# Optimization experiments

Hardware: AMD Instinct MI355X
Metric: run time of the kernel (lower is better)

## Reference

```python
import jax, jax.numpy as jnp
import numpy as np

NUM_NODES = 64
NUM_FEATURES = 256
OUTPUT_DIM = 256
BATCH_GRAPHS = 4096
TOTAL_ROWS = NUM_NODES * BATCH_GRAPHS


def setup_inputs() -> dict:
    key = jax.random.key(0)
    kx, kw = jax.random.split(key)
    x = jax.random.normal(kx, (TOTAL_ROWS, NUM_FEATURES), dtype=jnp.float32)
    # row i belongs to graph i // NUM_NODES (matches stride-num_nodes indexing in the module)
    batch = jnp.arange(TOTAL_ROWS, dtype=jnp.int64) // NUM_NODES
    # per-node linear weights: mlp[inode] is o3.Linear(256x0e -> 256x0e), bias-free
    W = jax.random.normal(kw, (NUM_NODES, NUM_FEATURES, OUTPUT_DIM), dtype=jnp.float32)
    return {"x": x, "batch": batch, "W": W}


def reference(x, batch, W):
    # x: [B*num_nodes, F]; W: [num_nodes, F, O]
    num_nodes, F, _ = W.shape
    B = x.shape[0] // num_nodes
    # node_features_reshape: out[b, :, inode] = x[inode + b*num_nodes] == reshape(B, num_nodes, F)
    xr = x.reshape(B, num_nodes, F)
    scale = 1.0 / jnp.sqrt(jnp.asarray(F, dtype=x.dtype))  # o3.Linear path normalization
    out = jnp.einsum("bnf,nfo->bno", xr, W) * scale  # per-node batched GEMM
    # scatter back: outs[inode + b*num_nodes] = out[b, inode] == reshape
    return out.reshape(B * num_nodes, -1)
```

## Files before the change

### kernel.cpp

```cpp
#include <hip/hip_runtime.h>
#include <stdint.h>

#define NODES   64
#define FDIM    256
#define ODIM    256
#define BGRAPH  4096
#define TROWS   (NODES * BGRAPH)

#define BM 64
#define BN 256
#define BK 32

typedef short  bf16x8  __attribute__((ext_vector_type(8)));
typedef float  floatx4 __attribute__((ext_vector_type(4)));

__device__ inline unsigned short f2bf(float f) {
    unsigned int u = __float_as_uint(f);
    return (unsigned short)((u + 0x7fffu + ((u >> 16) & 1u)) >> 16);
}

__global__ __launch_bounds__(256) void transpose_w(const float* __restrict__ W,
                                                   unsigned short* __restrict__ Wt) {
    __shared__ unsigned short t[64][65];
    const int node = blockIdx.y;
    const int tf = (blockIdx.x >> 2) << 6;
    const int to = (blockIdx.x & 3) << 6;
    const int tid = threadIdx.x;
    const float* Wn = W + node * (FDIM * ODIM);
#pragma unroll
    for (int i = 0; i < 16; ++i) {
        int flat = i * 256 + tid;
        int r = flat >> 6, c = flat & 63;
        float v = Wn[(tf + r) * ODIM + (to + c)] * 0.0625f;
        t[c][r] = f2bf(v);
    }
    __syncthreads();
    unsigned short* Wtn = Wt + node * (FDIM * ODIM);
#pragma unroll
    for (int i = 0; i < 16; ++i) {
        int flat = i * 256 + tid;
        int r = flat >> 6, c = flat & 63;
        Wtn[(to + r) * FDIM + (tf + c)] = t[r][c];
    }
}

__global__ __launch_bounds__(512, 4) void gemm_node(const float* __restrict__ x,
                                                    const unsigned short* __restrict__ Wt,
                                                    float* __restrict__ out) {
    __shared__ __align__(16) unsigned short As[BM * 256];
    __shared__ __align__(16) unsigned short Bs[2][BN * BK];

    const int bid  = blockIdx.x;
    const int xcd  = bid & 7;
    const int jj   = bid >> 3;
    const int node = xcd * 8 + (jj & 7);
    const int mblk = jj >> 3;
    const int b0   = mblk * BM;

    const int tid  = threadIdx.x;
    const int lane = tid & 63;
    const int wave = tid >> 6;
    const int wm   = wave >> 2;
    const int wn   = wave & 3;
    const int l15  = lane & 15;
    const int l4   = lane >> 4;

    const float* xblk = x + ((size_t)b0 * NODES + node) * FDIM;
    const unsigned short* wt_node = Wt + (size_t)node * (ODIM * FDIM);

#pragma unroll
    for (int j = 0; j < 2; ++j) {
        const int slot_base = (wave * 2 + j) * 64;
        const int s = slot_base + lane;
        const int o = s >> 2, c = s & 3;
        const int jg = c ^ ((o >> 1) & 3);
        const unsigned short* g = wt_node + (size_t)o * FDIM + jg * 8;
        __builtin_amdgcn_global_load_lds(
            (const __attribute__((address_space(1))) void*)g,
            (__attribute__((address_space(3))) void*)(&Bs[0][slot_base * 8]),
            16, 0, 0);
    }

#pragma unroll
    for (int i = 0; i < 8; ++i) {
        const int q = i * 512 + tid;
        const int r = q >> 6, ch = q & 63;
        const float4 v = *(const float4*)(xblk + (size_t)r * (NODES * FDIM) + ch * 4);
        ushort4 p;
        p.x = f2bf(v.x); p.y = f2bf(v.y); p.z = f2bf(v.z); p.w = f2bf(v.w);
        const int slot = (ch >> 1) ^ (r & 7);
        *(ushort4*)(&As[r * 256 + slot * 8 + (ch & 1) * 4]) = p;
    }
    __syncthreads();

    floatx4 acc[2][4] = {};

#pragma unroll
    for (int kt = 0; kt < 8; ++kt) {
        const int cur = kt & 1, nxt = cur ^ 1;

        if (kt < 7) {
            const int k1 = (kt + 1) * BK;
#pragma unroll
            for (int j = 0; j < 2; ++j) {
                const int slot_base = (wave * 2 + j) * 64;
                const int s = slot_base + lane;
                const int o = s >> 2, c = s & 3;
                const int jg = c ^ ((o >> 1) & 3);
                const unsigned short* g = wt_node + (size_t)o * FDIM + k1 + jg * 8;
                __builtin_amdgcn_global_load_lds(
                    (const __attribute__((address_space(1))) void*)g,
                    (__attribute__((address_space(3))) void*)(&Bs[nxt][slot_base * 8]),
                    16, 0, 0);
            }
        }

        bf16x8 a[2], b[4];
#pragma unroll
        for (int mi = 0; mi < 2; ++mi) {
            const int m = wm * 32 + mi * 16 + l15;
            const int slot = (kt * 4 + l4) ^ (m & 7);
            a[mi] = *(const bf16x8*)(&As[m * 256 + slot * 8]);
        }
#pragma unroll
        for (int ni = 0; ni < 4; ++ni) {
            const int n = wn * 64 + ni * 16 + l15;
            b[ni] = *(const bf16x8*)(&Bs[cur][n * 32 + (l4 ^ ((n >> 1) & 3)) * 8]);
        }

#pragma unroll
        for (int mi = 0; mi < 2; ++mi)
#pragma unroll
            for (int ni = 0; ni < 4; ++ni)
                acc[mi][ni] = __builtin_amdgcn_mfma_f32_16x16x32_bf16(a[mi], b[ni], acc[mi][ni], 0, 0, 0);

        if (kt < 7) __syncthreads();
    }

    float* outblk = out + ((size_t)b0 * NODES + node) * ODIM;
#pragma unroll
    for (int mi = 0; mi < 2; ++mi) {
        const int row_base = wm * 32 + mi * 16 + l4 * 4;
#pragma unroll
        for (int ni = 0; ni < 4; ++ni) {
            const int col = wn * 64 + ni * 16 + l15;
#pragma unroll
            for (int r = 0; r < 4; ++r) {
                outblk[(size_t)(row_base + r) * (NODES * ODIM) + col] = acc[mi][ni][r];
            }
        }
    }
}

__global__ __launch_bounds__(256) void naive_kernel(const float* __restrict__ x,
                                                    const float* __restrict__ W,
                                                    float* __restrict__ out) {
    __shared__ float xs[FDIM];
    const int row = blockIdx.x;
    const int node = row & (NODES - 1);
    const int o = threadIdx.x;
    xs[o] = x[(size_t)row * FDIM + o];
    __syncthreads();
    const float* Wn = W + (size_t)node * FDIM * ODIM;
    float s = 0.f;
#pragma unroll 8
    for (int f = 0; f < FDIM; ++f) s += xs[f] * Wn[(size_t)f * ODIM + o];
    out[(size_t)row * ODIM + o] = s * 0.0625f;
}

extern "C" void kernel_launch(void* const* d_in, const int* in_sizes, int n_in,
                              void* d_out, int out_size, void* d_ws, size_t ws_size,
                              hipStream_t stream) {
    const float* x = (const float*)d_in[0];
    const float* W = (const float*)d_in[2];
    float* out = (float*)d_out;

    const size_t wt_bytes = (size_t)NODES * ODIM * FDIM * sizeof(unsigned short);
    if (ws_size >= wt_bytes) {
        unsigned short* Wt = (unsigned short*)d_ws;
        transpose_w<<<dim3(16, NODES), 256, 0, stream>>>(W, Wt);
        gemm_node<<<dim3((BGRAPH / BM) * NODES), 512, 0, stream>>>(x, Wt, out);
    } else {
        naive_kernel<<<dim3(TROWS), 256, 0, stream>>>(x, W, out);
    }
}
```

Before: 455.6 us.

## Load W fragments directly from global into registers, drop LDS B staging

Removes the shared-memory double buffer for the weight tile. Each lane now loads its MFMA B fragments straight from global memory into registers, with an even/odd register double buffer, which also removes the per-k-step __syncthreads. This cuts LDS traffic, LDS footprint and block-wide barriers. In exchange, each wave issues many small strided global loads, and the two wm waves that share a wn column fetch the same W data redundantly (served by cache). Global latency may also be less well hidden.

```diff
diff --git a/kernel.cpp b/kernel.cpp
--- a/kernel.cpp
+++ b/kernel.cpp
@@ -48,7 +48,6 @@
                                                     const unsigned short* __restrict__ Wt,
                                                     float* __restrict__ out) {
     __shared__ __align__(16) unsigned short As[BM * 256];
-    __shared__ __align__(16) unsigned short Bs[2][BN * BK];
 
     const int bid  = blockIdx.x;
     const int xcd  = bid & 7;
@@ -68,18 +67,12 @@
     const float* xblk = x + ((size_t)b0 * NODES + node) * FDIM;
     const unsigned short* wt_node = Wt + (size_t)node * (ODIM * FDIM);
 
+    const unsigned short* bbase = wt_node + (size_t)(wn * 64 + l15) * FDIM + l4 * 8;
+
+    bf16x8 be[4], bo[4];
 #pragma unroll
-    for (int j = 0; j < 2; ++j) {
-        const int slot_base = (wave * 2 + j) * 64;
-        const int s = slot_base + lane;
-        const int o = s >> 2, c = s & 3;
-        const int jg = c ^ ((o >> 1) & 3);
-        const unsigned short* g = wt_node + (size_t)o * FDIM + jg * 8;
-        __builtin_amdgcn_global_load_lds(
-            (const __attribute__((address_space(1))) void*)g,
-            (__attribute__((address_space(3))) void*)(&Bs[0][slot_base * 8]),
-            16, 0, 0);
-    }
+    for (int ni = 0; ni < 4; ++ni)
+        be[ni] = *(const bf16x8*)(bbase + ni * 16 * FDIM);
 
 #pragma unroll
     for (int i = 0; i < 8; ++i) {
@@ -97,44 +90,30 @@
 
 #pragma unroll
     for (int kt = 0; kt < 8; ++kt) {
-        const int cur = kt & 1, nxt = cur ^ 1;
-
         if (kt < 7) {
             const int k1 = (kt + 1) * BK;
 #pragma unroll
-            for (int j = 0; j < 2; ++j) {
-                const int slot_base = (wave * 2 + j) * 64;
-                const int s = slot_base + lane;
-                const int o = s >> 2, c = s & 3;
-                const int jg = c ^ ((o >> 1) & 3);
-                const unsigned short* g = wt_node + (size_t)o * FDIM + k1 + jg * 8;
-                __builtin_amdgcn_global_load_lds(
-                    (const __attribute__((address_space(1))) void*)g,
-                    (__attribute__((address_space(3))) void*)(&Bs[nxt][slot_base * 8]),
-                    16, 0, 0);
+            for (int ni = 0; ni < 4; ++ni) {
+                bf16x8 v = *(const bf16x8*)(bbase + ni * 16 * FDIM + k1);
+                if (kt & 1) be[ni] = v; else bo[ni] = v;
             }
         }
 
-        bf16x8 a[2], b[4];
+        bf16x8 a[2];
 #pragma unroll
         for (int mi = 0; mi < 2; ++mi) {
             const int m = wm * 32 + mi * 16 + l15;
             const int slot = (kt * 4 + l4) ^ (m & 7);
             a[mi] = *(const bf16x8*)(&As[m * 256 + slot * 8]);
         }
-#pragma unroll
-        for (int ni = 0; ni < 4; ++ni) {
-            const int n = wn * 64 + ni * 16 + l15;
-            b[ni] = *(const bf16x8*)(&Bs[cur][n * 32 + (l4 ^ ((n >> 1) & 3)) * 8]);
-        }
 
 #pragma unroll
         for (int mi = 0; mi < 2; ++mi)
 #pragma unroll
-            for (int ni = 0; ni < 4; ++ni)
-                acc[mi][ni] = __builtin_amdgcn_mfma_f32_16x16x32_bf16(a[mi], b[ni], acc[mi][ni], 0, 0, 0);
-
-        if (kt < 7) __syncthreads();
+            for (int ni = 0; ni < 4; ++ni) {
+                const bf16x8 bf = (kt & 1) ? bo[ni] : be[ni];
+                acc[mi][ni] = __builtin_amdgcn_mfma_f32_16x16x32_bf16(a[mi], bf, acc[mi][ni], 0, 0, 0);
+            }
     }
 
     float* outblk = out + ((size_t)b0 * NODES + node) * ODIM;
```

After: 522.0 us. +14.6%, slower.
